# Optimization experiments

Hardware: AMD Instinct MI355X
Metric: run time of the kernel (lower is better)

Reference implementation:

```python
import jax, jax.numpy as jnp
import numpy as np

K = 512   # number of automaton states
S = 64    # segment vocabulary size
BSZ = 512 # batch of sequences
T = 64    # sequence length
A_SCALE = 0.02  # keeps recurrence spectral radius < 1 for numerical stability


def setup_inputs() -> dict:
    key = jax.random.key(0)
    kA, kB, kC, kP, kT = jax.random.split(key, 5)
    A = A_SCALE * jax.random.normal(kA, (K, K), dtype=jnp.float32)
    B = jax.random.normal(kB, (K, S), dtype=jnp.float32)
    C = jax.random.normal(kC, (S, K), dtype=jnp.float32)
    pi_params = jax.random.normal(kP, (S, K), dtype=jnp.float32)
    init = jnp.zeros((K,), dtype=jnp.float32).at[0].set(1.0)  # default e_0 init
    tokens = jax.random.randint(kT, (BSZ, T), 0, S, dtype=jnp.int32)
    return {"A": A, "B": B, "C": C, "pi_params": pi_params, "init": init, "tokens": tokens}


def reference(A, B, C, pi_params, init, tokens):
    # Real-semiring SSM forward recurrence (SSM.forward with float dtype):
    #   u[t]    = phi[input[t]]                (phi = eye(S) -> one-hot, realized as gathers)
    #   proj[t] = u[t] @ pi                    (tier gating, sigmoid-constrained to [0,1])
    #   x[t+1]  = (1 - proj[t]) * x[t] + proj[t] * (A @ x[t] + B @ u[t])
    #   y[t]    = (C * pi) @ x[t]              (predicts token t from pre-update state)
    # log-likelihood per sequence = sum_t log_softmax(y[t])[token_t]
    pi = jax.nn.sigmoid(pi_params)          # (S, K)
    C_eff = C * pi                          # (S, K)
    Bt = B.T                                # (S, K): Bt[tok] == B @ one_hot(tok)
    bsz = tokens.shape[0]
    x0 = jnp.broadcast_to(init, (bsz, init.shape[0]))  # (B, K)

    def step(x, tok):
        proj = pi[tok]                      # (B, K)
        update = x @ A.T + Bt[tok]          # (B, K)
        x_new = (1.0 - proj) * x + proj * update
        logits = x @ C_eff.T                # (B, S): y[t] from x[t] (pre-update)
        logp = jax.nn.log_softmax(logits, axis=-1)
        ll_t = jnp.take_along_axis(logp, tok[:, None], axis=-1)[:, 0]  # (B,)
        return x_new, ll_t

    _, lls = jax.lax.scan(step, x0, tokens.T)  # lls: (T, B)
    return lls.sum(0)                          # (B,) per-sequence log-likelihood
```

## Files before the change

kernel.cpp:

```cpp
#include <hip/hip_runtime.h>

#define K_DIM 512
#define S_DIM 64
#define T_LEN 64
#define BW    16
#define NWG   32

typedef float f32x4 __attribute__((ext_vector_type(4)));
typedef float f32x2 __attribute__((ext_vector_type(2)));
typedef long  i64x2 __attribute__((ext_vector_type(2)));

__device__ __forceinline__ char f2fp8(float f) {
    return (char)__builtin_amdgcn_cvt_pk_fp8_f32(f, f, 0, false);
}

__global__ void ssm_prep(const float* __restrict__ A, const float* __restrict__ B,
                         const float* __restrict__ C, const float* __restrict__ Pp,
                         char* __restrict__ A8, char* __restrict__ C8,
                         f32x2* __restrict__ PPB) {
    int i = blockIdx.x * blockDim.x + threadIdx.x;
    int stride = gridDim.x * blockDim.x;
    for (int idx = i; idx < K_DIM * K_DIM; idx += stride)
        A8[idx] = f2fp8(A[idx]);
    for (int idx = i; idx < S_DIM * K_DIM; idx += stride) {
        int s = idx >> 9;
        int k = idx & (K_DIM - 1);
        float p = 1.0f / (1.0f + expf(-Pp[idx]));
        C8[idx] = f2fp8(C[idx] * p);
        PPB[idx] = (f32x2){p, p * B[k * S_DIM + s]};
    }
}

#define MFMA8(xj, aj, acc) acc = __builtin_amdgcn_mfma_f32_16x16x32_fp8_fp8(xj, aj, acc, 0, 0, 0)

#define LOADM(m) \
    i64x2 ga_##m = *(const i64x2*)(a8P0 + (m) * 64); \
    i64x2 gb_##m = *(const i64x2*)(a8P1 + (m) * 64); \
    i64x2 gc_##m = *(const i64x2*)(a8P2 + (m) * 64); \
    i64x2 gd_##m = *(const i64x2*)(a8P3 + (m) * 64);

#define COMPM(m) { \
    i64x2 xv = *(const i64x2*)&Xb8[lr][(m) * 64 + 16 * lg]; \
    MFMA8(xv[0], ga_##m[0], acc0); MFMA8(xv[1], ga_##m[1], acc0); \
    MFMA8(xv[0], gb_##m[0], acc1); MFMA8(xv[1], gb_##m[1], acc1); \
    MFMA8(xv[0], gc_##m[0], acc2); MFMA8(xv[1], gc_##m[1], acc2); \
    MFMA8(xv[0], gd_##m[0], acc3); MFMA8(xv[1], gd_##m[1], acc3); }

#define COMPML(m) { \
    i64x2 xv = *(const i64x2*)&Xb8[lr][(m) * 64 + 16 * lg]; \
    i64x2 f0 = *(const i64x2*)&Aq8[w][(m) - 4][0][l][0]; \
    i64x2 f1 = *(const i64x2*)&Aq8[w][(m) - 4][1][l][0]; \
    i64x2 f2 = *(const i64x2*)&Aq8[w][(m) - 4][2][l][0]; \
    i64x2 f3 = *(const i64x2*)&Aq8[w][(m) - 4][3][l][0]; \
    MFMA8(xv[0], f0[0], acc0); MFMA8(xv[1], f0[1], acc0); \
    MFMA8(xv[0], f1[0], acc1); MFMA8(xv[1], f1[1], acc1); \
    MFMA8(xv[0], f2[0], acc2); MFMA8(xv[1], f2[1], acc2); \
    MFMA8(xv[0], f3[0], acc3); MFMA8(xv[1], f3[1], acc3); }

#define LBAR asm volatile("s_waitcnt lgkmcnt(0)\ns_barrier" ::: "memory")

__global__ __launch_bounds__(512) __attribute__((amdgpu_waves_per_eu(2, 2)))
void ssm_main(
    const char*  __restrict__ A8,
    const char*  __restrict__ C8,
    const f32x2* __restrict__ PPB,
    const float* __restrict__ init,
    const int*   __restrict__ tokens,
    float*       __restrict__ out)
{
    __shared__ char  Aq8[8][4][4][64][16];
    __shared__ char  Xb8[BW][528];
    __shared__ float Lg[2][BW][68];
    __shared__ int   tokS[BW][T_LEN];

    const int tid = threadIdx.x;
    const int w  = tid >> 6;
    const int l  = tid & 63;
    const int lg = l >> 4;
    const int lr = l & 15;
    const int b0 = blockIdx.x * BW;

    for (int idx = tid; idx < BW * T_LEN; idx += 512) {
        int r = idx >> 6, t = idx & 63;
        tokS[r][t] = tokens[(b0 + r) * T_LEN + t];
    }
    for (int idx = tid; idx < BW * K_DIM; idx += 512) {
        int r = idx >> 9, k = idx & (K_DIM - 1);
        Xb8[r][k] = f2fp8(init[k]);
    }
    for (int idx = tid; idx < 8192; idx += 512) {
        int w2 = idx >> 10, rem = idx & 1023;
        int m2 = rem >> 8, rem2 = rem & 255;
        int q2 = rem2 >> 6, l2 = rem2 & 63;
        *(i64x2*)&Aq8[w2][m2][q2][l2][0] =
            *(const i64x2*)(A8 + (w2 * 64 + q2 * 16 + (l2 & 15)) * K_DIM
                            + (4 + m2) * 64 + (l2 >> 4) * 16);
    }
    float xm[4][4];
    #pragma unroll
    for (int nt = 0; nt < 4; ++nt) {
        float iv = init[w * 64 + nt * 16 + lr];
        #pragma unroll
        for (int e = 0; e < 4; ++e) xm[nt][e] = iv;
    }

    const int sq = w & 3;
    const int kh = w >> 2;

    const char* a8P0 = A8 + (w * 64 +      lr) * K_DIM + 16 * lg;
    const char* a8P1 = A8 + (w * 64 + 16 + lr) * K_DIM + 16 * lg;
    const char* a8P2 = A8 + (w * 64 + 32 + lr) * K_DIM + 16 * lg;
    const char* a8P3 = A8 + (w * 64 + 48 + lr) * K_DIM + 16 * lg;
    const char* c8P  = C8 + (sq * 16 + lr) * K_DIM + kh * 256 + 16 * lg;

    float llacc = 0.0f;
    __syncthreads();

    for (int t = 0; t < T_LEN; ++t) {
        LOADM(0) LOADM(1)

        f32x4 lga = {0.f, 0.f, 0.f, 0.f};
        #pragma unroll
        for (int j = 0; j < 4; ++j) {
            i64x2 cv = *(const i64x2*)(c8P + j * 64);
            i64x2 xv = *(const i64x2*)&Xb8[lr][kh * 256 + j * 64 + 16 * lg];
            MFMA8(xv[0], cv[0], lga);
            MFMA8(xv[1], cv[1], lga);
        }
        #pragma unroll
        for (int e = 0; e < 4; ++e)
            Lg[kh][4 * lg + e][sq * 16 + lr] = lga[e];

        f32x4 acc0 = {0.f, 0.f, 0.f, 0.f};
        f32x4 acc1 = {0.f, 0.f, 0.f, 0.f};
        f32x4 acc2 = {0.f, 0.f, 0.f, 0.f};
        f32x4 acc3 = {0.f, 0.f, 0.f, 0.f};
        COMPM(0)  LOADM(2)
        COMPM(1)  LOADM(3)
        COMPM(2)
        COMPM(3)
        int mytok[4];
        #pragma unroll
        for (int e = 0; e < 4; ++e) mytok[e] = tokS[4 * lg + e][t];
        f32x2 ppv[4][4];
        #pragma unroll
        for (int nt = 0; nt < 4; ++nt) {
            int k = w * 64 + nt * 16 + lr;
            #pragma unroll
            for (int e = 0; e < 4; ++e)
                ppv[nt][e] = PPB[mytok[e] * K_DIM + k];
        }
        COMPML(4) COMPML(5) COMPML(6) COMPML(7)
        LBAR;

        #pragma unroll
        for (int nt = 0; nt < 4; ++nt) {
            int k = w * 64 + nt * 16 + lr;
            #pragma unroll
            for (int e = 0; e < 4; ++e) {
                float a  = (nt == 0) ? acc0[e] : (nt == 1) ? acc1[e]
                         : (nt == 2) ? acc2[e] : acc3[e];
                float nx = xm[nt][e] + ppv[nt][e][0] * (a - xm[nt][e]) + ppv[nt][e][1];
                xm[nt][e] = nx;
                Xb8[4 * lg + e][k] = f2fp8(nx);
            }
        }
        if (w < 4) {
            int b = w * 4 + (l >> 4);
            int i = l & 15;
            float v[4];
            #pragma unroll
            for (int c = 0; c < 4; ++c)
                v[c] = Lg[0][b][i * 4 + c] + Lg[1][b][i * 4 + c];
            float m = fmaxf(fmaxf(v[0], v[1]), fmaxf(v[2], v[3]));
            m = fmaxf(m, __shfl_xor(m, 1));
            m = fmaxf(m, __shfl_xor(m, 2));
            m = fmaxf(m, __shfl_xor(m, 4));
            m = fmaxf(m, __shfl_xor(m, 8));
            float sum = expf(v[0] - m) + expf(v[1] - m) + expf(v[2] - m) + expf(v[3] - m);
            sum += __shfl_xor(sum, 1);
            sum += __shfl_xor(sum, 2);
            sum += __shfl_xor(sum, 4);
            sum += __shfl_xor(sum, 8);
            int tok = tokS[b][t];
            float sel = (i == (tok >> 2)) ? v[tok & 3] : 0.0f;
            sel += __shfl_xor(sel, 1);
            sel += __shfl_xor(sel, 2);
            sel += __shfl_xor(sel, 4);
            sel += __shfl_xor(sel, 8);
            llacc += sel - m - logf(sum);
        }
        LBAR;
    }

    if (w < 4 && (l & 15) == 0)
        out[b0 + w * 4 + (l >> 4)] = llacc;
}

extern "C" void kernel_launch(void* const* d_in, const int* in_sizes, int n_in,
                              void* d_out, int out_size, void* d_ws, size_t ws_size,
                              hipStream_t stream) {
    const float* A  = (const float*)d_in[0];
    const float* B  = (const float*)d_in[1];
    const float* C  = (const float*)d_in[2];
    const float* Pp = (const float*)d_in[3];
    const float* init = (const float*)d_in[4];
    const int* tokens = (const int*)d_in[5];
    float* out = (float*)d_out;

    char*  A8  = (char*)d_ws;
    char*  C8  = (char*)d_ws + 262144;
    f32x2* PPB = (f32x2*)((char*)d_ws + 294912);

    ssm_prep<<<256, 256, 0, stream>>>(A, B, C, Pp, A8, C8, PPB);
    ssm_main<<<NWG, 512, 0, stream>>>(A8, C8, PPB, init, tokens, out);
}
```

Baseline: 177.7 us.

## Prefetch next-step A and C fragments across barrier; spread softmax over all waves

The C fragments and the first two A column blocks are loaded into registers at the end of each step (before the barrier), so the next iteration's logits and first MFMAs no longer wait on global-memory latency. The log-softmax reduction now runs on all 8 waves, with 32 lanes per sequence handling 2 logits each, instead of only 4 waves with 16 lanes each. This shortens the critical path of the serial recurrence, but it raises register pressure, which could cause spills under the 2-waves-per-EU limit.

```diff
diff --git a/kernel.cpp b/kernel.cpp
--- a/kernel.cpp
+++ b/kernel.cpp
@@ -46,6 +46,13 @@
     MFMA8(xv[0], gc_##m[0], acc2); MFMA8(xv[1], gc_##m[1], acc2); \
     MFMA8(xv[0], gd_##m[0], acc3); MFMA8(xv[1], gd_##m[1], acc3); }
 
+#define COMPC(pa, pb, pc, pd, m) { \
+    i64x2 xv = *(const i64x2*)&Xb8[lr][(m) * 64 + 16 * lg]; \
+    MFMA8(xv[0], pa[0], acc0); MFMA8(xv[1], pa[1], acc0); \
+    MFMA8(xv[0], pb[0], acc1); MFMA8(xv[1], pb[1], acc1); \
+    MFMA8(xv[0], pc[0], acc2); MFMA8(xv[1], pc[1], acc2); \
+    MFMA8(xv[0], pd[0], acc3); MFMA8(xv[1], pd[1], acc3); }
+
 #define COMPML(m) { \
     i64x2 xv = *(const i64x2*)&Xb8[lr][(m) * 64 + 16 * lg]; \
     i64x2 f0 = *(const i64x2*)&Aq8[w][(m) - 4][0][l][0]; \
@@ -56,6 +63,15 @@
     MFMA8(xv[0], f1[0], acc1); MFMA8(xv[1], f1[1], acc1); \
     MFMA8(xv[0], f2[0], acc2); MFMA8(xv[1], f2[1], acc2); \
     MFMA8(xv[0], f3[0], acc3); MFMA8(xv[1], f3[1], acc3); }
+
+#define CARRY() do { \
+    cv0 = *(const i64x2*)(c8P);        cv1 = *(const i64x2*)(c8P +  64); \
+    cv2 = *(const i64x2*)(c8P + 128);  cv3 = *(const i64x2*)(c8P + 192); \
+    p0a = *(const i64x2*)(a8P0);       p0b = *(const i64x2*)(a8P1); \
+    p0c = *(const i64x2*)(a8P2);       p0d = *(const i64x2*)(a8P3); \
+    p1a = *(const i64x2*)(a8P0 + 64);  p1b = *(const i64x2*)(a8P1 + 64); \
+    p1c = *(const i64x2*)(a8P2 + 64);  p1d = *(const i64x2*)(a8P3 + 64); \
+} while (0)
 
 #define LBAR asm volatile("s_waitcnt lgkmcnt(0)\ns_barrier" ::: "memory")
 
@@ -113,19 +129,26 @@
     const char* a8P3 = A8 + (w * 64 + 48 + lr) * K_DIM + 16 * lg;
     const char* c8P  = C8 + (sq * 16 + lr) * K_DIM + kh * 256 + 16 * lg;
 
+    i64x2 cv0, cv1, cv2, cv3;
+    i64x2 p0a, p0b, p0c, p0d, p1a, p1b, p1c, p1d;
+    CARRY();
+
     float llacc = 0.0f;
     __syncthreads();
 
     for (int t = 0; t < T_LEN; ++t) {
-        LOADM(0) LOADM(1)
+        LOADM(2) LOADM(3)
 
         f32x4 lga = {0.f, 0.f, 0.f, 0.f};
-        #pragma unroll
-        for (int j = 0; j < 4; ++j) {
-            i64x2 cv = *(const i64x2*)(c8P + j * 64);
-            i64x2 xv = *(const i64x2*)&Xb8[lr][kh * 256 + j * 64 + 16 * lg];
-            MFMA8(xv[0], cv[0], lga);
-            MFMA8(xv[1], cv[1], lga);
+        {
+            i64x2 xv0 = *(const i64x2*)&Xb8[lr][kh * 256 +   0 + 16 * lg];
+            MFMA8(xv0[0], cv0[0], lga); MFMA8(xv0[1], cv0[1], lga);
+            i64x2 xv1 = *(const i64x2*)&Xb8[lr][kh * 256 +  64 + 16 * lg];
+            MFMA8(xv1[0], cv1[0], lga); MFMA8(xv1[1], cv1[1], lga);
+            i64x2 xv2 = *(const i64x2*)&Xb8[lr][kh * 256 + 128 + 16 * lg];
+            MFMA8(xv2[0], cv2[0], lga); MFMA8(xv2[1], cv2[1], lga);
+            i64x2 xv3 = *(const i64x2*)&Xb8[lr][kh * 256 + 192 + 16 * lg];
+            MFMA8(xv3[0], cv3[0], lga); MFMA8(xv3[1], cv3[1], lga);
         }
         #pragma unroll
         for (int e = 0; e < 4; ++e)
@@ -135,8 +158,8 @@
         f32x4 acc1 = {0.f, 0.f, 0.f, 0.f};
         f32x4 acc2 = {0.f, 0.f, 0.f, 0.f};
         f32x4 acc3 = {0.f, 0.f, 0.f, 0.f};
-        COMPM(0)  LOADM(2)
-        COMPM(1)  LOADM(3)
+        COMPC(p0a, p0b, p0c, p0d, 0)
+        COMPC(p1a, p1b, p1c, p1d, 1)
         COMPM(2)
         COMPM(3)
         int mytok[4];
@@ -165,36 +188,38 @@
                 Xb8[4 * lg + e][k] = f2fp8(nx);
             }
         }
-        if (w < 4) {
-            int b = w * 4 + (l >> 4);
-            int i = l & 15;
-            float v[4];
-            #pragma unroll
-            for (int c = 0; c < 4; ++c)
-                v[c] = Lg[0][b][i * 4 + c] + Lg[1][b][i * 4 + c];
-            float m = fmaxf(fmaxf(v[0], v[1]), fmaxf(v[2], v[3]));
+        CARRY();
+        {
+            int b = w * 2 + (l >> 5);
+            int i = l & 31;
+            float v0 = Lg[0][b][i * 2]     + Lg[1][b][i * 2];
+            float v1 = Lg[0][b][i * 2 + 1] + Lg[1][b][i * 2 + 1];
+            float m = fmaxf(v0, v1);
             m = fmaxf(m, __shfl_xor(m, 1));
             m = fmaxf(m, __shfl_xor(m, 2));
             m = fmaxf(m, __shfl_xor(m, 4));
             m = fmaxf(m, __shfl_xor(m, 8));
-            float sum = expf(v[0] - m) + expf(v[1] - m) + expf(v[2] - m) + expf(v[3] - m);
+            m = fmaxf(m, __shfl_xor(m, 16));
+            float sum = expf(v0 - m) + expf(v1 - m);
             sum += __shfl_xor(sum, 1);
             sum += __shfl_xor(sum, 2);
             sum += __shfl_xor(sum, 4);
             sum += __shfl_xor(sum, 8);
+            sum += __shfl_xor(sum, 16);
             int tok = tokS[b][t];
-            float sel = (i == (tok >> 2)) ? v[tok & 3] : 0.0f;
+            float sel = (i == (tok >> 1)) ? ((tok & 1) ? v1 : v0) : 0.0f;
             sel += __shfl_xor(sel, 1);
             sel += __shfl_xor(sel, 2);
             sel += __shfl_xor(sel, 4);
             sel += __shfl_xor(sel, 8);
+            sel += __shfl_xor(sel, 16);
             llacc += sel - m - logf(sum);
         }
         LBAR;
     }
 
-    if (w < 4 && (l & 15) == 0)
-        out[b0 + w * 4 + (l >> 4)] = llacc;
+    if ((l & 31) == 0)
+        out[b0 + w * 2 + (l >> 5)] = llacc;
 }
 
 extern "C" void kernel_launch(void* const* d_in, const int* in_sizes, int n_in,
```

Result: slower. 256.2 us (+44.2%).
